# Performance work log

Hardware: AMD Instinct MI355X
Metric: run time of the kernel (lower is better)

Reference implementation:

```python
import jax, jax.numpy as jnp
import numpy as np

B, IN, OUT = 4096, 2048, 2048
GRID_SIZE, SPLINE_ORDER, Q_LEVELS = 5, 3, 64
N_COEFF = GRID_SIZE + SPLINE_ORDER  # 8


def setup_inputs() -> dict:
    key = jax.random.key(0)
    k1, k2, k3 = jax.random.split(key, 3)
    x = jax.random.uniform(k1, (B, IN), dtype=jnp.float32, minval=-1.0, maxval=1.0)
    # kaiming_uniform_(a=sqrt(5)) -> bound = 1/sqrt(in_features)
    bound = 1.0 / np.sqrt(IN)
    base_weight = jax.random.uniform(k2, (OUT, IN), dtype=jnp.float32, minval=-bound, maxval=bound)
    spline_weight = 0.1 * jax.random.normal(k3, (OUT, IN, N_COEFF), dtype=jnp.float32)
    h = 2.0 / GRID_SIZE
    grid_1d = jnp.arange(-SPLINE_ORDER, GRID_SIZE + SPLINE_ORDER + 1, dtype=jnp.float32) * h - 1.0
    grid = jnp.broadcast_to(grid_1d, (IN, grid_1d.shape[0]))  # [in, grid+2k+1]=[in,12]
    return {"x": x, "base_weight": base_weight, "spline_weight": spline_weight, "grid": grid}


def b_splines(x, grid, k):
    # x: [b, in], grid: [in, n_knots] -> bases: [b, in, n_knots-1-k]
    xe = x[:, :, None]           # [b, in, 1]
    g = grid[None, :, :]         # [1, in, n_knots]
    bases = ((xe >= g[:, :, :-1]) & (xe < g[:, :, 1:])).astype(x.dtype)
    for p in range(1, k + 1):
        t_i = g[:, :, : -1 - p]
        t_i_p = g[:, :, p:-1]
        term1 = (xe - t_i) / (t_i_p - t_i + 1e-8) * bases[:, :, :-1]
        t_i_1 = g[:, :, 1:-p]
        t_i_p_1 = g[:, :, p + 1:]
        term2 = (t_i_p_1 - xe) / (t_i_p_1 - t_i_1 + 1e-8) * bases[:, :, 1:]
        bases = term1 + term2
    return bases


def quantize_ste(w, levels):
    scale = levels / 2.0
    q = jnp.round(w * scale) / scale
    # straight-through estimator: identity gradient
    return w + jax.lax.stop_gradient(q - w)


def reference(x, base_weight, spline_weight, grid) -> jnp.ndarray:
    base_output = x @ base_weight.T                       # [b, out]
    basis = b_splines(x, grid, SPLINE_ORDER)              # [b, in, 8]
    q_weight = quantize_ste(spline_weight, Q_LEVELS)      # [out, in, 8]
    spline_output = jnp.einsum('bic,oic->bo', basis, q_weight)
    return base_output + spline_output
```

## Files before the change

### kernel.cpp

```cpp
#include <hip/hip_runtime.h>
#include <stdint.h>

#define B_DIM   4096
#define IN_DIM  2048
#define OUT_DIM 2048
#define NC      8
#define KTOT    (IN_DIM * NC)
#define KHALF   (KTOT / 2)

typedef __bf16 bf16x8 __attribute__((ext_vector_type(8)));
typedef float  floatx4 __attribute__((ext_vector_type(4)));
typedef unsigned short ushortx8 __attribute__((ext_vector_type(8)));

__device__ __forceinline__ unsigned short f2bf(float f) {
  unsigned int u = __float_as_uint(f);
  return (unsigned short)((u + 0x7FFFu + ((u >> 16) & 1u)) >> 16);
}

__device__ __forceinline__ void load_lds16(const void* g, void* l) {
  __builtin_amdgcn_global_load_lds(
      (const __attribute__((address_space(1))) void*)g,
      (__attribute__((address_space(3))) void*)l, 16, 0, 0);
}

__global__ __launch_bounds__(256) void build_A(const float* __restrict__ x,
                                               const float* __restrict__ grid,
                                               unsigned short* __restrict__ Abuf) {
  __shared__ float g[12];
  __shared__ float rec[3][12];
  int t = threadIdx.x;
  if (t < 12) g[t] = grid[t];
  __syncthreads();
  if (t < 36) {
    int p = t / 12 + 1, j = t % 12;
    if (j + p <= 11) rec[p - 1][j] = 1.0f / (g[j + p] - g[j] + 1e-8f);
  }
  __syncthreads();
  int idx = blockIdx.x * 256 + t;
  float xv = x[idx];
  float bs[11];
#pragma unroll
  for (int j = 0; j < 11; ++j)
    bs[j] = (xv >= g[j] && xv < g[j + 1]) ? 1.0f : 0.0f;
#pragma unroll
  for (int p = 1; p <= 3; ++p) {
#pragma unroll
    for (int j = 0; j + p < 11; ++j) {
      float t1 = (xv - g[j])         * rec[p - 1][j];
      float t2 = (g[j + p + 1] - xv) * rec[p - 1][j + 1];
      bs[j] = t1 * bs[j] + t2 * bs[j + 1];
    }
  }
  ushortx8 pk;
#pragma unroll
  for (int c = 0; c < 8; ++c) pk[c] = f2bf(bs[c]);
  *(ushortx8*)&Abuf[(size_t)idx * 8] = pk;
}

__global__ __launch_bounds__(256) void build_B(const float* __restrict__ sw,
                                               const float* __restrict__ bw,
                                               unsigned short* __restrict__ Bbuf) {
  int idx = blockIdx.x * 256 + threadIdx.x;
  const float4* swv = (const float4*)sw;
  float4 w0 = swv[(size_t)idx * 2];
  float4 w1 = swv[(size_t)idx * 2 + 1];
  float bwv = bw[idx];
  ushortx8 pk;
  pk[0] = f2bf(fmaf(-1.4f, bwv, rintf(w0.x * 32.f) * 0.03125f));
  pk[1] = f2bf(fmaf(-1.0f, bwv, rintf(w0.y * 32.f) * 0.03125f));
  pk[2] = f2bf(fmaf(-0.6f, bwv, rintf(w0.z * 32.f) * 0.03125f));
  pk[3] = f2bf(fmaf(-0.2f, bwv, rintf(w0.w * 32.f) * 0.03125f));
  pk[4] = f2bf(fmaf( 0.2f, bwv, rintf(w1.x * 32.f) * 0.03125f));
  pk[5] = f2bf(fmaf( 0.6f, bwv, rintf(w1.y * 32.f) * 0.03125f));
  pk[6] = f2bf(fmaf( 1.0f, bwv, rintf(w1.z * 32.f) * 0.03125f));
  pk[7] = f2bf(fmaf( 1.4f, bwv, rintf(w1.w * 32.f) * 0.03125f));
  *(ushortx8*)&Bbuf[(size_t)idx * 8] = pk;
}

__global__ __launch_bounds__(512, 2) void gemm256(const unsigned short* __restrict__ A,
                                                  const unsigned short* __restrict__ Bm,
                                                  float* __restrict__ C0,
                                                  float* __restrict__ C1,
                                                  int klen) {
  __shared__ unsigned short lds[65536];

  const int tid  = threadIdx.x;
  const int wid  = tid >> 6;
  const int lane = tid & 63;
  const int wr = wid >> 2, wc = wid & 3;
  const int lm = lane & 15, lq = lane >> 4;

  const int s01 = (lq ^ (lm & 3)) * 8;
  const int sk0 = ((lm >> 2) & 1) * 32;
  const int sk1 = 32 - sk0;

  int lid = blockIdx.y * gridDim.x + blockIdx.x;
  lid = (lid & 7) * 16 + (lid >> 3);
  const int col0  = (lid & 7) * 256;
  const int row0  = (lid >> 3) * 256;
  const int kbase = blockIdx.z * klen;

  const int srow = lane >> 3;
  const int scg  = ((lane & 7) ^ srow) * 8;

  size_t offA[2][2], offB[2][2];
  int    dstA[2][2], dstB[2][2];
#pragma unroll
  for (int m = 0; m < 2; ++m)
#pragma unroll
    for (int q = 0; q < 2; ++q) {
      int rs = q * 128 + m * 64 + wid * 8;
      offA[m][q] = (size_t)(row0 + rs + srow) * KTOT + scg;
      dstA[m][q] = rs * 64;
    }
#pragma unroll
  for (int n = 0; n < 2; ++n)
#pragma unroll
    for (int q = 0; q < 2; ++q) {
      int g  = q * 8 + wid;
      int rs = ((g >> 2) * 2 + n) * 32 + (g & 3) * 8;
      offB[n][q] = (size_t)(col0 + rs + srow) * KTOT + scg;
      dstB[n][q] = rs * 64;
    }

#define STAGE_A(m, d, kp) do {                                                   \
    load_lds16(A + offA[m][0] + (kp), &lds[(d) * 32768 + dstA[m][0]]);           \
    load_lds16(A + offA[m][1] + (kp), &lds[(d) * 32768 + dstA[m][1]]);           \
  } while (0)
#define STAGE_B(n, d, kp) do {                                                   \
    load_lds16(Bm + offB[n][0] + (kp), &lds[(d) * 32768 + 16384 + dstB[n][0]]);  \
    load_lds16(Bm + offB[n][1] + (kp), &lds[(d) * 32768 + 16384 + dstB[n][1]]);  \
  } while (0)

#define VM4 asm volatile("s_waitcnt vmcnt(4)" ::: "memory")
#define VM2 asm volatile("s_waitcnt vmcnt(2)" ::: "memory")
#define VM0 asm volatile("s_waitcnt vmcnt(0)" ::: "memory")
#define NOWAIT ((void)0)

  const unsigned short* ldsA0 = lds + (wr * 128 + lm) * 64 + s01;
  const unsigned short* ldsB0 = lds + 16384 + (wc * 64 + lm) * 64 + s01;

  floatx4 acc[8][4];
#pragma unroll
  for (int i = 0; i < 8; ++i)
#pragma unroll
    for (int j = 0; j < 4; ++j) acc[i][j] = floatx4{0.f, 0.f, 0.f, 0.f};

  STAGE_A(0, 0, kbase);
  STAGE_B(0, 0, kbase);
  STAGE_B(1, 0, kbase);
  STAGE_A(1, 0, kbase);
  asm volatile("s_waitcnt vmcnt(4)" ::: "memory");
  __builtin_amdgcn_s_barrier();
  __builtin_amdgcn_sched_barrier(0);

#define RD_A(pA, mh) do {                                                        \
    _Pragma("unroll") for (int m_ = 0; m_ < 4; ++m_) {                           \
      af_[m_][0] = *(const bf16x8*)((pA) + (mh) * 4096 + m_ * 1024 + sk0);       \
      af_[m_][1] = *(const bf16x8*)((pA) + (mh) * 4096 + m_ * 1024 + sk1);       \
    }                                                                            \
  } while (0)
#define RD_B(pB, dst, nh) do {                                                   \
    _Pragma("unroll") for (int n_ = 0; n_ < 2; ++n_) {                           \
      dst[n_][0] = *(const bf16x8*)((pB) + (nh) * 2048 + n_ * 1024 + sk0);       \
      dst[n_][1] = *(const bf16x8*)((pB) + (nh) * 2048 + n_ * 1024 + sk1);       \
    }                                                                            \
  } while (0)
#define MM(mh, nh, bfr)                                                          \
    _Pragma("unroll") for (int m_ = 0; m_ < 4; ++m_)                             \
      _Pragma("unroll") for (int n_ = 0; n_ < 2; ++n_)                           \
        _Pragma("unroll") for (int k_ = 0; k_ < 2; ++k_)                         \
          acc[(mh) * 4 + m_][(nh) * 2 + n_] =                                    \
              __builtin_amdgcn_mfma_f32_16x16x32_bf16(                           \
                  af_[m_][k_], bfr[n_][k_],                                      \
                  acc[(mh) * 4 + m_][(nh) * 2 + n_], 0, 0, 0)
#define BARX do { __builtin_amdgcn_s_barrier();                                  \
    asm volatile("s_waitcnt lgkmcnt(0)" ::: "memory");                           \
    __builtin_amdgcn_sched_barrier(0); } while (0)
#define MMP(mh, nh, bfr) do { __builtin_amdgcn_s_setprio(1);                     \
    MM(mh, nh, bfr); __builtin_amdgcn_s_setprio(0); } while (0)

  const int NT = klen / 64;
  int kp = kbase + 64;
  for (int t = 0; t < NT - 1; ++t) {
    const int dB_ = t & 1, dN_ = dB_ ^ 1;
    const unsigned short* pA = ldsA0 + dB_ * 32768;
    const unsigned short* pB = ldsB0 + dB_ * 32768;
    bf16x8 af_[4][2], bf0_[2][2], bf1_[2][2];
    RD_A(pA, 0); RD_B(pB, bf0_, 0); STAGE_A(0, dN_, kp); VM4; BARX;
    MMP(0, 0, bf0_);
    RD_B(pB, bf1_, 1); STAGE_B(0, dN_, kp); VM4; BARX;
    MMP(0, 1, bf1_);
    RD_A(pA, 1); STAGE_B(1, dN_, kp); BARX;
    MMP(1, 1, bf1_);
    STAGE_A(1, dN_, kp); VM4; BARX;
    MMP(1, 0, bf0_);
    kp += 64;
  }
  {
    const int dB_ = (NT - 1) & 1;
    const unsigned short* pA = ldsA0 + dB_ * 32768;
    const unsigned short* pB = ldsB0 + dB_ * 32768;
    bf16x8 af_[4][2], bf0_[2][2], bf1_[2][2];
    RD_A(pA, 0); RD_B(pB, bf0_, 0); VM2; BARX;
    MMP(0, 0, bf0_);
    RD_B(pB, bf1_, 1); VM0; BARX;
    MMP(0, 1, bf1_);
    RD_A(pA, 1); BARX;
    MMP(1, 1, bf1_);
    MMP(1, 0, bf0_);
  }
#undef RD_A
#undef RD_B
#undef MM
#undef MMP
#undef BARX
#undef STAGE_A
#undef STAGE_B
#undef VM4
#undef VM2
#undef VM0
#undef NOWAIT

  float* __restrict__ C = blockIdx.z ? C1 : C0;
#pragma unroll
  for (int mf = 0; mf < 8; ++mf) {
    int rr = row0 + wr * 128 + mf * 16 + lq * 4;
#pragma unroll
    for (int nf = 0; nf < 4; ++nf) {
      int cc = col0 + wc * 64 + nf * 16 + lm;
#pragma unroll
      for (int q = 0; q < 4; ++q)
        C[(size_t)(rr + q) * OUT_DIM + cc] = acc[mf][nf][q];
    }
  }
}

__global__ __launch_bounds__(256) void reduce_add(float* __restrict__ out,
                                                  const float* __restrict__ part) {
  int i = blockIdx.x * 256 + threadIdx.x;
  float4 a = ((const float4*)out)[i];
  float4 p = ((const float4*)part)[i];
  a.x += p.x; a.y += p.y; a.z += p.z; a.w += p.w;
  ((float4*)out)[i] = a;
}

extern "C" void kernel_launch(void* const* d_in, const int* in_sizes, int n_in,
                              void* d_out, int out_size, void* d_ws, size_t ws_size,
                              hipStream_t stream) {
  const float* x    = (const float*)d_in[0];
  const float* bw   = (const float*)d_in[1];
  const float* sw   = (const float*)d_in[2];
  const float* grid = (const float*)d_in[3];
  float* out = (float*)d_out;

  unsigned short* Abuf = (unsigned short*)d_ws;
  unsigned short* Bbuf = Abuf + (size_t)B_DIM * KTOT;
  float* Cpart = (float*)(Bbuf + (size_t)OUT_DIM * KTOT);
  const size_t need_split =
      ((size_t)B_DIM + OUT_DIM) * KTOT * 2 + (size_t)B_DIM * OUT_DIM * 4;
  const bool split = ws_size >= need_split;

  hipLaunchKernelGGL(build_A, dim3(B_DIM * IN_DIM / 256), dim3(256), 0, stream,
                     x, grid, Abuf);
  hipLaunchKernelGGL(build_B, dim3(OUT_DIM * IN_DIM / 256), dim3(256), 0, stream,
                     sw, bw, Bbuf);
  if (split) {
    hipLaunchKernelGGL(gemm256, dim3(OUT_DIM / 256, B_DIM / 256, 2), dim3(512),
                       0, stream, Abuf, Bbuf, out, Cpart, KHALF);
    hipLaunchKernelGGL(reduce_add, dim3(B_DIM * OUT_DIM / 4 / 256), dim3(256),
                       0, stream, out, Cpart);
  } else {
    hipLaunchKernelGGL(gemm256, dim3(OUT_DIM / 256, B_DIM / 256, 1), dim3(512),
                       0, stream, Abuf, Bbuf, out, (float*)nullptr, KTOT);
  }
}
```

Baseline: 513.7 us.

## Merge A/B prep kernels and re-pipeline GEMM LDS reads with finer waitcnts

The two preprocessing kernels become a single launch that branches on block index, which removes one kernel launch and the gap between them. The GEMM main loop is rescheduled so that LDS fragment reads are split per k-half, with partial lgkmcnt waits letting the first MFMA half start before every read lands. The B fragments for the next tile are prefetched at the end of each iteration, and barriers no longer force lgkmcnt(0). This targets LDS latency stalls inside the compute loop. The price is more delicate wait-count bookkeeping and a long-lived bf0_ register set carried across iterations.

```diff
diff --git a/kernel.cpp b/kernel.cpp
--- a/kernel.cpp
+++ b/kernel.cpp
@@ -7,6 +7,8 @@
 #define NC      8
 #define KTOT    (IN_DIM * NC)
 #define KHALF   (KTOT / 2)
+#define NBLK_A  (B_DIM * IN_DIM / 256)
+#define NBLK_B  (OUT_DIM * IN_DIM / 256)
 
 typedef __bf16 bf16x8 __attribute__((ext_vector_type(8)));
 typedef float  floatx4 __attribute__((ext_vector_type(4)));
@@ -23,58 +25,59 @@
       (__attribute__((address_space(3))) void*)l, 16, 0, 0);
 }
 
-__global__ __launch_bounds__(256) void build_A(const float* __restrict__ x,
-                                               const float* __restrict__ grid,
-                                               unsigned short* __restrict__ Abuf) {
-  __shared__ float g[12];
-  __shared__ float rec[3][12];
+__global__ __launch_bounds__(256) void build_AB(const float* __restrict__ x,
+                                                const float* __restrict__ grid,
+                                                const float* __restrict__ sw,
+                                                const float* __restrict__ bw,
+                                                unsigned short* __restrict__ Abuf,
+                                                unsigned short* __restrict__ Bbuf) {
   int t = threadIdx.x;
-  if (t < 12) g[t] = grid[t];
-  __syncthreads();
-  if (t < 36) {
-    int p = t / 12 + 1, j = t % 12;
-    if (j + p <= 11) rec[p - 1][j] = 1.0f / (g[j + p] - g[j] + 1e-8f);
-  }
-  __syncthreads();
-  int idx = blockIdx.x * 256 + t;
-  float xv = x[idx];
-  float bs[11];
-#pragma unroll
-  for (int j = 0; j < 11; ++j)
-    bs[j] = (xv >= g[j] && xv < g[j + 1]) ? 1.0f : 0.0f;
-#pragma unroll
-  for (int p = 1; p <= 3; ++p) {
-#pragma unroll
-    for (int j = 0; j + p < 11; ++j) {
-      float t1 = (xv - g[j])         * rec[p - 1][j];
-      float t2 = (g[j + p + 1] - xv) * rec[p - 1][j + 1];
-      bs[j] = t1 * bs[j] + t2 * bs[j + 1];
-    }
-  }
-  ushortx8 pk;
-#pragma unroll
-  for (int c = 0; c < 8; ++c) pk[c] = f2bf(bs[c]);
-  *(ushortx8*)&Abuf[(size_t)idx * 8] = pk;
-}
-
-__global__ __launch_bounds__(256) void build_B(const float* __restrict__ sw,
-                                               const float* __restrict__ bw,
-                                               unsigned short* __restrict__ Bbuf) {
-  int idx = blockIdx.x * 256 + threadIdx.x;
-  const float4* swv = (const float4*)sw;
-  float4 w0 = swv[(size_t)idx * 2];
-  float4 w1 = swv[(size_t)idx * 2 + 1];
-  float bwv = bw[idx];
-  ushortx8 pk;
-  pk[0] = f2bf(fmaf(-1.4f, bwv, rintf(w0.x * 32.f) * 0.03125f));
-  pk[1] = f2bf(fmaf(-1.0f, bwv, rintf(w0.y * 32.f) * 0.03125f));
-  pk[2] = f2bf(fmaf(-0.6f, bwv, rintf(w0.z * 32.f) * 0.03125f));
-  pk[3] = f2bf(fmaf(-0.2f, bwv, rintf(w0.w * 32.f) * 0.03125f));
-  pk[4] = f2bf(fmaf( 0.2f, bwv, rintf(w1.x * 32.f) * 0.03125f));
-  pk[5] = f2bf(fmaf( 0.6f, bwv, rintf(w1.y * 32.f) * 0.03125f));
-  pk[6] = f2bf(fmaf( 1.0f, bwv, rintf(w1.z * 32.f) * 0.03125f));
-  pk[7] = f2bf(fmaf( 1.4f, bwv, rintf(w1.w * 32.f) * 0.03125f));
-  *(ushortx8*)&Bbuf[(size_t)idx * 8] = pk;
+  if (blockIdx.x < NBLK_A) {
+    __shared__ float g[12];
+    __shared__ float rec[3][12];
+    if (t < 12) g[t] = grid[t];
+    __syncthreads();
+    if (t < 36) {
+      int p = t / 12 + 1, j = t % 12;
+      if (j + p <= 11) rec[p - 1][j] = 1.0f / (g[j + p] - g[j] + 1e-8f);
+    }
+    __syncthreads();
+    int idx = blockIdx.x * 256 + t;
+    float xv = x[idx];
+    float bs[11];
+#pragma unroll
+    for (int j = 0; j < 11; ++j)
+      bs[j] = (xv >= g[j] && xv < g[j + 1]) ? 1.0f : 0.0f;
+#pragma unroll
+    for (int p = 1; p <= 3; ++p) {
+#pragma unroll
+      for (int j = 0; j + p < 11; ++j) {
+        float t1 = (xv - g[j])         * rec[p - 1][j];
+        float t2 = (g[j + p + 1] - xv) * rec[p - 1][j + 1];
+        bs[j] = t1 * bs[j] + t2 * bs[j + 1];
+      }
+    }
+    ushortx8 pk;
+#pragma unroll
+    for (int c = 0; c < 8; ++c) pk[c] = f2bf(bs[c]);
+    *(ushortx8*)&Abuf[(size_t)idx * 8] = pk;
+  } else {
+    int idx = (blockIdx.x - NBLK_A) * 256 + t;
+    const float4* swv = (const float4*)sw;
+    float4 w0 = swv[(size_t)idx * 2];
+    float4 w1 = swv[(size_t)idx * 2 + 1];
+    float bwv = bw[idx];
+    ushortx8 pk;
+    pk[0] = f2bf(fmaf(-1.4f, bwv, rintf(w0.x * 32.f) * 0.03125f));
+    pk[1] = f2bf(fmaf(-1.0f, bwv, rintf(w0.y * 32.f) * 0.03125f));
+    pk[2] = f2bf(fmaf(-0.6f, bwv, rintf(w0.z * 32.f) * 0.03125f));
+    pk[3] = f2bf(fmaf(-0.2f, bwv, rintf(w0.w * 32.f) * 0.03125f));
+    pk[4] = f2bf(fmaf( 0.2f, bwv, rintf(w1.x * 32.f) * 0.03125f));
+    pk[5] = f2bf(fmaf( 0.6f, bwv, rintf(w1.y * 32.f) * 0.03125f));
+    pk[6] = f2bf(fmaf( 1.0f, bwv, rintf(w1.z * 32.f) * 0.03125f));
+    pk[7] = f2bf(fmaf( 1.4f, bwv, rintf(w1.w * 32.f) * 0.03125f));
+    *(ushortx8*)&Bbuf[(size_t)idx * 8] = pk;
+  }
 }
 
 __global__ __launch_bounds__(512, 2) void gemm256(const unsigned short* __restrict__ A,
@@ -135,92 +138,117 @@
 #define VM4 asm volatile("s_waitcnt vmcnt(4)" ::: "memory")
 #define VM2 asm volatile("s_waitcnt vmcnt(2)" ::: "memory")
 #define VM0 asm volatile("s_waitcnt vmcnt(0)" ::: "memory")
-#define NOWAIT ((void)0)
+#define LG4 do { asm volatile("s_waitcnt lgkmcnt(4)" ::: "memory");              \
+                 __builtin_amdgcn_sched_barrier(0); } while (0)
+#define LG2 do { asm volatile("s_waitcnt lgkmcnt(2)" ::: "memory");              \
+                 __builtin_amdgcn_sched_barrier(0); } while (0)
+#define LG0 do { asm volatile("s_waitcnt lgkmcnt(0)" ::: "memory");              \
+                 __builtin_amdgcn_sched_barrier(0); } while (0)
+#define BARS do { __builtin_amdgcn_s_barrier();                                  \
+                  __builtin_amdgcn_sched_barrier(0); } while (0)
+#define SB0_ __builtin_amdgcn_sched_barrier(0)
+#define PRIO1 __builtin_amdgcn_s_setprio(1)
+#define PRIO0 __builtin_amdgcn_s_setprio(0)
 
   const unsigned short* ldsA0 = lds + (wr * 128 + lm) * 64 + s01;
   const unsigned short* ldsB0 = lds + 16384 + (wc * 64 + lm) * 64 + s01;
 
+#define RD_AK(pA, mh, kk) do {                                                   \
+    _Pragma("unroll") for (int m_ = 0; m_ < 4; ++m_)                             \
+      af_[m_][kk] = *(const bf16x8*)((pA) + (mh) * 4096 + m_ * 1024 +            \
+                                     ((kk) ? sk1 : sk0));                        \
+  } while (0)
+#define RD_BK(pB, dst, nh, kk) do {                                              \
+    _Pragma("unroll") for (int n_ = 0; n_ < 2; ++n_)                             \
+      dst[n_][kk] = *(const bf16x8*)((pB) + (nh) * 2048 + n_ * 1024 +            \
+                                     ((kk) ? sk1 : sk0));                        \
+  } while (0)
+#define MM8(mh, nh, bfr, kk)                                                     \
+    _Pragma("unroll") for (int m_ = 0; m_ < 4; ++m_)                             \
+      _Pragma("unroll") for (int n_ = 0; n_ < 2; ++n_)                           \
+        acc[(mh) * 4 + m_][(nh) * 2 + n_] =                                      \
+            __builtin_amdgcn_mfma_f32_16x16x32_bf16(                             \
+                af_[m_][kk], bfr[n_][kk],                                        \
+                acc[(mh) * 4 + m_][(nh) * 2 + n_], 0, 0, 0)
+
   floatx4 acc[8][4];
 #pragma unroll
   for (int i = 0; i < 8; ++i)
 #pragma unroll
     for (int j = 0; j < 4; ++j) acc[i][j] = floatx4{0.f, 0.f, 0.f, 0.f};
+
+  bf16x8 bf0_[2][2];
 
   STAGE_A(0, 0, kbase);
   STAGE_B(0, 0, kbase);
   STAGE_B(1, 0, kbase);
   STAGE_A(1, 0, kbase);
-  asm volatile("s_waitcnt vmcnt(4)" ::: "memory");
-  __builtin_amdgcn_s_barrier();
-  __builtin_amdgcn_sched_barrier(0);
-
-#define RD_A(pA, mh) do {                                                        \
-    _Pragma("unroll") for (int m_ = 0; m_ < 4; ++m_) {                           \
-      af_[m_][0] = *(const bf16x8*)((pA) + (mh) * 4096 + m_ * 1024 + sk0);       \
-      af_[m_][1] = *(const bf16x8*)((pA) + (mh) * 4096 + m_ * 1024 + sk1);       \
-    }                                                                            \
-  } while (0)
-#define RD_B(pB, dst, nh) do {                                                   \
-    _Pragma("unroll") for (int n_ = 0; n_ < 2; ++n_) {                           \
-      dst[n_][0] = *(const bf16x8*)((pB) + (nh) * 2048 + n_ * 1024 + sk0);       \
-      dst[n_][1] = *(const bf16x8*)((pB) + (nh) * 2048 + n_ * 1024 + sk1);       \
-    }                                                                            \
-  } while (0)
-#define MM(mh, nh, bfr)                                                          \
-    _Pragma("unroll") for (int m_ = 0; m_ < 4; ++m_)                             \
-      _Pragma("unroll") for (int n_ = 0; n_ < 2; ++n_)                           \
-        _Pragma("unroll") for (int k_ = 0; k_ < 2; ++k_)                         \
-          acc[(mh) * 4 + m_][(nh) * 2 + n_] =                                    \
-              __builtin_amdgcn_mfma_f32_16x16x32_bf16(                           \
-                  af_[m_][k_], bfr[n_][k_],                                      \
-                  acc[(mh) * 4 + m_][(nh) * 2 + n_], 0, 0, 0)
-#define BARX do { __builtin_amdgcn_s_barrier();                                  \
-    asm volatile("s_waitcnt lgkmcnt(0)" ::: "memory");                           \
-    __builtin_amdgcn_sched_barrier(0); } while (0)
-#define MMP(mh, nh, bfr) do { __builtin_amdgcn_s_setprio(1);                     \
-    MM(mh, nh, bfr); __builtin_amdgcn_s_setprio(0); } while (0)
+  VM4;
+  BARS;
+  RD_BK(ldsB0, bf0_, 0, 0); RD_BK(ldsB0, bf0_, 0, 1);
 
   const int NT = klen / 64;
   int kp = kbase + 64;
   for (int t = 0; t < NT - 1; ++t) {
     const int dB_ = t & 1, dN_ = dB_ ^ 1;
-    const unsigned short* pA = ldsA0 + dB_ * 32768;
-    const unsigned short* pB = ldsB0 + dB_ * 32768;
-    bf16x8 af_[4][2], bf0_[2][2], bf1_[2][2];
-    RD_A(pA, 0); RD_B(pB, bf0_, 0); STAGE_A(0, dN_, kp); VM4; BARX;
-    MMP(0, 0, bf0_);
-    RD_B(pB, bf1_, 1); STAGE_B(0, dN_, kp); VM4; BARX;
-    MMP(0, 1, bf1_);
-    RD_A(pA, 1); STAGE_B(1, dN_, kp); BARX;
-    MMP(1, 1, bf1_);
-    STAGE_A(1, dN_, kp); VM4; BARX;
-    MMP(1, 0, bf0_);
+    const unsigned short* pA  = ldsA0 + dB_ * 32768;
+    const unsigned short* pB  = ldsB0 + dB_ * 32768;
+    const unsigned short* pBn = ldsB0 + dN_ * 32768;
+    bf16x8 af_[4][2], bf1_[2][2];
+    BARS;
+    RD_AK(pA, 0, 0); SB0_; RD_AK(pA, 0, 1);
+    STAGE_A(0, dN_, kp);
+    LG4; PRIO1; MM8(0, 0, bf0_, 0); LG0; MM8(0, 0, bf0_, 1); PRIO0;
+    VM4;
+    BARS;
+    RD_BK(pB, bf1_, 1, 0); SB0_; RD_BK(pB, bf1_, 1, 1);
+    STAGE_B(0, dN_, kp);
+    LG2; PRIO1; MM8(0, 1, bf1_, 0); LG0; MM8(0, 1, bf1_, 1); PRIO0;
+    VM4;
+    BARS;
+    RD_AK(pA, 1, 0); SB0_; RD_AK(pA, 1, 1);
+    STAGE_B(1, dN_, kp);
+    LG4; PRIO1; MM8(1, 1, bf1_, 0); LG0; MM8(1, 1, bf1_, 1); PRIO0;
+    VM2;
+    BARS;
+    STAGE_A(1, dN_, kp);
+    PRIO1; MM8(1, 0, bf0_, 0); MM8(1, 0, bf0_, 1); PRIO0;
+    RD_BK(pBn, bf0_, 0, 0); RD_BK(pBn, bf0_, 0, 1);
     kp += 64;
   }
   {
     const int dB_ = (NT - 1) & 1;
     const unsigned short* pA = ldsA0 + dB_ * 32768;
     const unsigned short* pB = ldsB0 + dB_ * 32768;
-    bf16x8 af_[4][2], bf0_[2][2], bf1_[2][2];
-    RD_A(pA, 0); RD_B(pB, bf0_, 0); VM2; BARX;
-    MMP(0, 0, bf0_);
-    RD_B(pB, bf1_, 1); VM0; BARX;
-    MMP(0, 1, bf1_);
-    RD_A(pA, 1); BARX;
-    MMP(1, 1, bf1_);
-    MMP(1, 0, bf0_);
-  }
-#undef RD_A
-#undef RD_B
-#undef MM
-#undef MMP
-#undef BARX
+    bf16x8 af_[4][2], bf1_[2][2];
+    BARS;
+    RD_AK(pA, 0, 0); SB0_; RD_AK(pA, 0, 1);
+    LG4; PRIO1; MM8(0, 0, bf0_, 0); LG0; MM8(0, 0, bf0_, 1); PRIO0;
+    VM2;
+    BARS;
+    RD_BK(pB, bf1_, 1, 0); SB0_; RD_BK(pB, bf1_, 1, 1);
+    LG2; PRIO1; MM8(0, 1, bf1_, 0); LG0; MM8(0, 1, bf1_, 1); PRIO0;
+    VM0;
+    BARS;
+    RD_AK(pA, 1, 0); SB0_; RD_AK(pA, 1, 1);
+    LG4; PRIO1; MM8(1, 1, bf1_, 0); LG0; MM8(1, 1, bf1_, 1); PRIO0;
+    PRIO1; MM8(1, 0, bf0_, 0); MM8(1, 0, bf0_, 1); PRIO0;
+  }
+#undef RD_AK
+#undef RD_BK
+#undef MM8
 #undef STAGE_A
 #undef STAGE_B
 #undef VM4
 #undef VM2
 #undef VM0
-#undef NOWAIT
+#undef LG4
+#undef LG2
+#undef LG0
+#undef BARS
+#undef SB0_
+#undef PRIO1
+#undef PRIO0
 
   float* __restrict__ C = blockIdx.z ? C1 : C0;
 #pragma unroll
@@ -261,10 +289,8 @@
       ((size_t)B_DIM + OUT_DIM) * KTOT * 2 + (size_t)B_DIM * OUT_DIM * 4;
   const bool split = ws_size >= need_split;
 
-  hipLaunchKernelGGL(build_A, dim3(B_DIM * IN_DIM / 256), dim3(256), 0, stream,
-                     x, grid, Abuf);
-  hipLaunchKernelGGL(build_B, dim3(OUT_DIM * IN_DIM / 256), dim3(256), 0, stream,
-                     sw, bw, Bbuf);
+  hipLaunchKernelGGL(build_AB, dim3(NBLK_A + NBLK_B), dim3(256), 0, stream,
+                     x, grid, sw, bw, Abuf, Bbuf);
   if (split) {
     hipLaunchKernelGGL(gemm256, dim3(OUT_DIM / 256, B_DIM / 256, 2), dim3(512),
                        0, stream, Abuf, Bbuf, out, Cpart, KHALF);
```

Result: no change. 506.1 us (-1.5%).
